# Kernel tuning notes

Measured on AMD Instinct MI355X. Metric: run time of the kernel, lower is better.

Reference implementation:

```python
import jax, jax.numpy as jnp
import numpy as np

L_MAX = 3
N_MAX = 8
N_PSEUDO = 4
N_SPECIES = 4
CUTOFF = 5.0


def real_sph_harm(u):
    # u: [E,3] unit vectors -> real spherical harmonics, l=0..3, [E,16]
    x, y, z = u[:, 0], u[:, 1], u[:, 2]
    x2, y2, z2 = x * x, y * y, z * z
    Y = [
        0.28209479177387814 * jnp.ones_like(x),
        0.4886025119029199 * y,
        0.4886025119029199 * z,
        0.4886025119029199 * x,
        1.0925484305920792 * x * y,
        1.0925484305920792 * y * z,
        0.31539156525252005 * (3.0 * z2 - 1.0),
        1.0925484305920792 * x * z,
        0.5462742152960396 * (x2 - y2),
        0.5900435899266435 * y * (3.0 * x2 - y2),
        2.890611442640554 * x * y * z,
        0.4570457994644658 * y * (5.0 * z2 - 1.0),
        0.3731763325901154 * z * (5.0 * z2 - 3.0),
        0.4570457994644658 * x * (5.0 * z2 - 1.0),
        1.445305721320277 * z * (x2 - y2),
        0.5900435899266435 * x * (x2 - 3.0 * y2),
    ]
    return jnp.stack(Y, axis=-1)


def setup_inputs() -> dict:
    key = jax.random.key(0)
    k0, k1, k2, k3 = jax.random.split(key, 4)
    N, E = 20000, 320000
    positions = jax.random.normal(k0, (N, 3), jnp.float32) * 2.0
    cells = (30.0 * jnp.eye(3, dtype=jnp.float32))[None]  # [1,3,3]
    species = jax.random.randint(k1, (N,), 0, N_SPECIES)  # species indices
    edge_indices = jax.random.randint(k2, (2, E), 0, N)
    edge_shifts = jnp.zeros((E, 3), jnp.int32)
    species_embed = jax.random.normal(k3, (N_SPECIES, N_PSEUDO), jnp.float32)  # alchemical coupling
    radial_mu = jnp.linspace(0.0, CUTOFF, N_MAX).astype(jnp.float32)
    radial_sigma = jnp.full((1,), 0.6, jnp.float32)
    return {
        "positions": positions,
        "cells": cells,
        "species": species,
        "edge_indices": edge_indices,
        "edge_shifts": edge_shifts,
        "species_embed": species_embed,
        "radial_mu": radial_mu,
        "radial_sigma": radial_sigma,
    }


def reference(positions, cells, species, edge_indices, edge_shifts, species_embed, radial_mu, radial_sigma):
    i, j = edge_indices[0], edge_indices[1]
    # per-edge displacement with periodic shifts
    rij = positions[j] - positions[i] + edge_shifts.astype(positions.dtype) @ cells[0]  # [E,3]
    r = jnp.sqrt(jnp.sum(rij * rij, axis=-1) + 1e-12)  # [E]
    u = rij / r[:, None]
    # smooth cosine cutoff
    fcut = jnp.where(r < CUTOFF, 0.5 * (jnp.cos(jnp.pi * r / CUTOFF) + 1.0), 0.0)
    # radial expansion [E, n_max]
    sig = radial_sigma[0]
    R = jnp.exp(-((r[:, None] - radial_mu) ** 2) / (2.0 * sig * sig)) * fcut[:, None]
    # angular expansion [E, (l_max+1)^2]
    Y = real_sph_harm(u)
    # alchemical pseudo-species embedding of the neighbor species [E, P]
    ej = species_embed[species[j]]
    N = positions.shape[0]
    outs = []
    for l in range(L_MAX + 1):
        Yl = Y[:, l * l:(l + 1) * (l + 1)]  # [E, 2l+1]
        # per-edge spherical-expansion contribution, properties = (pseudo, n) flattened -> Q
        feat = jnp.einsum('em,ep,en->empn', Yl, ej, R).reshape(Yl.shape[0], 2 * l + 1, -1)
        # scatter edges to centers: c_{i,m,q}
        c = jax.ops.segment_sum(feat, i, num_segments=N)  # [N, 2l+1, Q]
        cg = (2 * l + 1) ** (-0.5)
        # power spectrum: cg * sum_m c_{imq} c_{imr}  -> [N, Q, Q]
        ps = cg * jnp.einsum('nmq,nmr->nqr', c, c)
        outs.append(ps.reshape(N, -1))
    return jnp.concatenate(outs, axis=-1)  # [N, sum_l Q^2] = [20000, 4096]
```

## Files before the change

kernel.cpp:

```cpp
#include <hip/hip_runtime.h>
#include <math.h>

#define NM       16
#define NQ       32
#define CUT      5.0f
#define CAP      96

typedef float v4f __attribute__((ext_vector_type(4)));

__global__ __launch_bounds__(256) void edge_bin_kernel(
    const float* __restrict__ pos,
    const float* __restrict__ cells,
    const int*   __restrict__ species,
    const int*   __restrict__ eidx,
    const int*   __restrict__ eshift,
    int*         __restrict__ counts,
    float4*      __restrict__ buckets,
    int E)
{
    const int e = blockIdx.x * blockDim.x + threadIdx.x;
    if (e >= E) return;

    const int i = eidx[e];
    const int j = eidx[E + e];

    float dx = pos[3 * j + 0] - pos[3 * i + 0];
    float dy = pos[3 * j + 1] - pos[3 * i + 1];
    float dz = pos[3 * j + 2] - pos[3 * i + 2];

    const int sx = eshift[3 * e + 0];
    const int sy = eshift[3 * e + 1];
    const int sz = eshift[3 * e + 2];
    dx += (float)sx * cells[0] + (float)sy * cells[3] + (float)sz * cells[6];
    dy += (float)sx * cells[1] + (float)sy * cells[4] + (float)sz * cells[7];
    dz += (float)sx * cells[2] + (float)sy * cells[5] + (float)sz * cells[8];

    const float r2 = dx * dx + dy * dy + dz * dz;
    if (r2 >= CUT * CUT) return;

    const int slot = atomicAdd(&counts[i], 1);
    if (slot < CAP)
        buckets[(size_t)i * CAP + slot] =
            make_float4(dx, dy, dz, __int_as_float(species[j]));
}

__global__ __launch_bounds__(256) void node_fused_kernel(
    const float4* __restrict__ buckets,
    const int*    __restrict__ counts,
    const float*  __restrict__ semb,
    const float*  __restrict__ mu,
    const float*  __restrict__ sigma,
    float*        __restrict__ out,
    int N)
{
    const int node = blockIdx.x;
    const int tid  = threadIdx.x;

    __shared__ float sY[64][17];
    __shared__ float sW[64][33];
    __shared__ __align__(16) float sc[NM * NQ];
    __shared__ float s_mu[8];
    __shared__ float s_semb[16];

    if (tid < 8)  s_mu[tid]   = mu[tid];
    if (tid < 16) s_semb[tid] = semb[tid];

    const float sig    = sigma[0];
    const float inv2s2 = -1.0f / (2.0f * sig * sig);

    const int cnt = min(counts[node], CAP);

    const int q  = tid & 31;
    const int m0 = tid >> 5;
    float acc0 = 0.0f, acc1 = 0.0f;

    for (int base = 0; base < cnt; base += 64) {
        const int nb = min(cnt - base, 64);
        __syncthreads();

        const int lane = tid & 63;
        const int half = tid >> 6;
        if (lane < nb && half < 2) {
            const float4 b = buckets[(size_t)node * CAP + base + lane];
            const float dx = b.x, dy = b.y, dz = b.z;
            const float r2 = dx * dx + dy * dy + dz * dz + 1e-12f;
            const float r  = sqrtf(r2);
            const float invr = 1.0f / r;
            if (half == 0) {
                const float x = dx * invr, y = dy * invr, z = dz * invr;
                const float x2 = x * x, y2 = y * y, z2 = z * z;
                float* Yr = sY[lane];
                Yr[0]  = 0.28209479177387814f;
                Yr[1]  = 0.4886025119029199f * y;
                Yr[2]  = 0.4886025119029199f * z;
                Yr[3]  = 0.4886025119029199f * x;
                Yr[4]  = 1.0925484305920792f * x * y;
                Yr[5]  = 1.0925484305920792f * y * z;
                Yr[6]  = 0.31539156525252005f * (3.0f * z2 - 1.0f);
                Yr[7]  = 1.0925484305920792f * x * z;
                Yr[8]  = 0.5462742152960396f * (x2 - y2);
                Yr[9]  = 0.5900435899266435f * y * (3.0f * x2 - y2);
                Yr[10] = 2.890611442640554f  * x * y * z;
                Yr[11] = 0.4570457994644658f * y * (5.0f * z2 - 1.0f);
                Yr[12] = 0.3731763325901154f * z * (5.0f * z2 - 3.0f);
                Yr[13] = 0.4570457994644658f * x * (5.0f * z2 - 1.0f);
                Yr[14] = 1.445305721320277f  * z * (x2 - y2);
                Yr[15] = 0.5900435899266435f * x * (x2 - 3.0f * y2);
            } else {
                const float fcut = 0.5f * (__cosf(0.62831853071795864f * r) + 1.0f);
                const int sj = __float_as_int(b.w);
                float R[8];
#pragma unroll
                for (int n = 0; n < 8; ++n) {
                    const float dr = r - s_mu[n];
                    R[n] = __expf(dr * dr * inv2s2) * fcut;
                }
                float* Wr = sW[lane];
#pragma unroll
                for (int p = 0; p < 4; ++p) {
                    const float ejp = s_semb[sj * 4 + p];
#pragma unroll
                    for (int n = 0; n < 8; ++n)
                        Wr[p * 8 + n] = ejp * R[n];
                }
            }
        }
        __syncthreads();

        for (int e = 0; e < nb; ++e) {
            const float w = sW[e][q];
            acc0 += sY[e][m0]     * w;
            acc1 += sY[e][m0 + 8] * w;
        }
    }

    __syncthreads();
    sc[m0 * NQ + q]       = acc0;
    sc[(m0 + 8) * NQ + q] = acc1;
    __syncthreads();

    const float cg[4] = {1.0f, 0.57735026918962576f,
                         0.44721359549995794f, 0.37796447300922723f};
    const int qc = tid >> 3;
    const int r8 = tid & 7;

    const v4f* sc4 = (const v4f*)sc;
    v4f* op = (v4f*)out + (size_t)node * 1024;

#pragma unroll
    for (int l = 0; l < 4; ++l) {
        const int mb = l * l;
        const int mc = 2 * l + 1;
        v4f s = {0.0f, 0.0f, 0.0f, 0.0f};
        for (int m = 0; m < mc; ++m) {
            const float a  = sc[(mb + m) * NQ + qc];
            const v4f   bv = sc4[(mb + m) * 8 + r8];
            s += a * bv;
        }
        s *= cg[l];
        __builtin_nontemporal_store(s, &op[l * 256 + tid]);
    }
}

extern "C" void kernel_launch(void* const* d_in, const int* in_sizes, int n_in,
                              void* d_out, int out_size, void* d_ws, size_t ws_size,
                              hipStream_t stream) {
    const float* pos     = (const float*)d_in[0];
    const float* cells   = (const float*)d_in[1];
    const int*   species = (const int*)  d_in[2];
    const int*   eidx    = (const int*)  d_in[3];
    const int*   eshift  = (const int*)  d_in[4];
    const float* semb    = (const float*)d_in[5];
    const float* mu      = (const float*)d_in[6];
    const float* sigma   = (const float*)d_in[7];
    float*       out     = (float*)d_out;

    const int N = in_sizes[0] / 3;
    const int E = in_sizes[3] / 2;

    float4* buckets = (float4*)d_ws;
    const size_t bucket_bytes = (size_t)N * CAP * sizeof(float4);
    int* counts = (int*)((char*)d_ws + bucket_bytes);

    hipMemsetAsync(counts, 0, (size_t)N * sizeof(int), stream);

    edge_bin_kernel<<<(E + 255) / 256, 256, 0, stream>>>(
        pos, cells, species, eidx, eshift, counts, buckets, E);

    node_fused_kernel<<<N, 256, 0, stream>>>(
        buckets, counts, semb, mu, sigma, out, N);
}
```

Baseline: 357.4 us.

## Map one wavefront per node and drop block-wide barriers in fused kernel

The node kernel now assigns one 64-lane wavefront to each node, with four nodes per 256-thread block, instead of a whole block per node. Each wave processes neighbours in chunks of 16. One lane per edge computes both the spherical harmonics and the radial/species weights into a per-wave LDS slot, and there is no __syncthreads. Accumulation uses vector registers, and the power-spectrum stage loads B rows into registers and reuses them across four output column groups. The goal is to remove barrier overhead and idle threads when nodes have few edges, at the cost of relying on implicit wave-level LDS ordering and running more of the work serially per lane.

```diff
diff --git a/kernel.cpp b/kernel.cpp
--- a/kernel.cpp
+++ b/kernel.cpp
@@ -5,6 +5,8 @@
 #define NQ       32
 #define CUT      5.0f
 #define CAP      96
+#define CHUNK    16
+#define SLOT     52
 
 typedef float v4f __attribute__((ext_vector_type(4)));
 
@@ -53,112 +55,118 @@
     float*        __restrict__ out,
     int N)
 {
-    const int node = blockIdx.x;
-    const int tid  = threadIdx.x;
-
-    __shared__ float sY[64][17];
-    __shared__ float sW[64][33];
-    __shared__ __align__(16) float sc[NM * NQ];
-    __shared__ float s_mu[8];
-    __shared__ float s_semb[16];
-
-    if (tid < 8)  s_mu[tid]   = mu[tid];
-    if (tid < 16) s_semb[tid] = semb[tid];
+    const int wid  = threadIdx.x >> 6;
+    const int lane = threadIdx.x & 63;
+    const int node = blockIdx.x * 4 + wid;
+    if (node >= N) return;
+
+    __shared__ __align__(16) float sE[4][CHUNK * SLOT];
+    float* wbase = sE[wid];
 
     const float sig    = sigma[0];
     const float inv2s2 = -1.0f / (2.0f * sig * sig);
 
     const int cnt = min(counts[node], CAP);
 
-    const int q  = tid & 31;
-    const int m0 = tid >> 5;
-    float acc0 = 0.0f, acc1 = 0.0f;
-
-    for (int base = 0; base < cnt; base += 64) {
-        const int nb = min(cnt - base, 64);
-        __syncthreads();
-
-        const int lane = tid & 63;
-        const int half = tid >> 6;
-        if (lane < nb && half < 2) {
+    const int q = lane & 31;
+    const int h = lane >> 5;
+    v4f acc0 = {0.f, 0.f, 0.f, 0.f};
+    v4f acc1 = {0.f, 0.f, 0.f, 0.f};
+
+    for (int base = 0; base < cnt; base += CHUNK) {
+        const int nb = min(cnt - base, CHUNK);
+
+        if (lane < nb) {
             const float4 b = buckets[(size_t)node * CAP + base + lane];
             const float dx = b.x, dy = b.y, dz = b.z;
             const float r2 = dx * dx + dy * dy + dz * dz + 1e-12f;
             const float r  = sqrtf(r2);
             const float invr = 1.0f / r;
-            if (half == 0) {
-                const float x = dx * invr, y = dy * invr, z = dz * invr;
-                const float x2 = x * x, y2 = y * y, z2 = z * z;
-                float* Yr = sY[lane];
-                Yr[0]  = 0.28209479177387814f;
-                Yr[1]  = 0.4886025119029199f * y;
-                Yr[2]  = 0.4886025119029199f * z;
-                Yr[3]  = 0.4886025119029199f * x;
-                Yr[4]  = 1.0925484305920792f * x * y;
-                Yr[5]  = 1.0925484305920792f * y * z;
-                Yr[6]  = 0.31539156525252005f * (3.0f * z2 - 1.0f);
-                Yr[7]  = 1.0925484305920792f * x * z;
-                Yr[8]  = 0.5462742152960396f * (x2 - y2);
-                Yr[9]  = 0.5900435899266435f * y * (3.0f * x2 - y2);
-                Yr[10] = 2.890611442640554f  * x * y * z;
-                Yr[11] = 0.4570457994644658f * y * (5.0f * z2 - 1.0f);
-                Yr[12] = 0.3731763325901154f * z * (5.0f * z2 - 3.0f);
-                Yr[13] = 0.4570457994644658f * x * (5.0f * z2 - 1.0f);
-                Yr[14] = 1.445305721320277f  * z * (x2 - y2);
-                Yr[15] = 0.5900435899266435f * x * (x2 - 3.0f * y2);
-            } else {
-                const float fcut = 0.5f * (__cosf(0.62831853071795864f * r) + 1.0f);
-                const int sj = __float_as_int(b.w);
-                float R[8];
-#pragma unroll
-                for (int n = 0; n < 8; ++n) {
-                    const float dr = r - s_mu[n];
-                    R[n] = __expf(dr * dr * inv2s2) * fcut;
-                }
-                float* Wr = sW[lane];
-#pragma unroll
-                for (int p = 0; p < 4; ++p) {
-                    const float ejp = s_semb[sj * 4 + p];
-#pragma unroll
-                    for (int n = 0; n < 8; ++n)
-                        Wr[p * 8 + n] = ejp * R[n];
-                }
+            const float x = dx * invr, y = dy * invr, z = dz * invr;
+            const float x2 = x * x, y2 = y * y, z2 = z * z;
+
+            v4f* slot4 = (v4f*)(wbase + lane * SLOT);
+            v4f Ya, Yb, Yc, Yd;
+            Ya[0] = 0.28209479177387814f;
+            Ya[1] = 0.4886025119029199f * y;
+            Ya[2] = 0.4886025119029199f * z;
+            Ya[3] = 0.4886025119029199f * x;
+            Yb[0] = 1.0925484305920792f * x * y;
+            Yb[1] = 1.0925484305920792f * y * z;
+            Yb[2] = 0.31539156525252005f * (3.0f * z2 - 1.0f);
+            Yb[3] = 1.0925484305920792f * x * z;
+            Yc[0] = 0.5462742152960396f * (x2 - y2);
+            Yc[1] = 0.5900435899266435f * y * (3.0f * x2 - y2);
+            Yc[2] = 2.890611442640554f  * x * y * z;
+            Yc[3] = 0.4570457994644658f * y * (5.0f * z2 - 1.0f);
+            Yd[0] = 0.3731763325901154f * z * (5.0f * z2 - 3.0f);
+            Yd[1] = 0.4570457994644658f * x * (5.0f * z2 - 1.0f);
+            Yd[2] = 1.445305721320277f  * z * (x2 - y2);
+            Yd[3] = 0.5900435899266435f * x * (x2 - 3.0f * y2);
+            slot4[0] = Ya; slot4[1] = Yb; slot4[2] = Yc; slot4[3] = Yd;
+
+            const float fcut = 0.5f * (__cosf(0.62831853071795864f * r) + 1.0f);
+            float Rf[8];
+#pragma unroll
+            for (int n = 0; n < 8; ++n) {
+                const float dr = r - mu[n];
+                Rf[n] = __expf(dr * dr * inv2s2) * fcut;
+            }
+            const int sj = __float_as_int(b.w);
+#pragma unroll
+            for (int p = 0; p < 4; ++p) {
+                const float ejp = semb[sj * 4 + p];
+                v4f w0, w1;
+#pragma unroll
+                for (int n = 0; n < 4; ++n) { w0[n] = ejp * Rf[n]; w1[n] = ejp * Rf[4 + n]; }
+                slot4[4 + 2 * p]     = w0;
+                slot4[4 + 2 * p + 1] = w1;
             }
         }
-        __syncthreads();
 
         for (int e = 0; e < nb; ++e) {
-            const float w = sW[e][q];
-            acc0 += sY[e][m0]     * w;
-            acc1 += sY[e][m0 + 8] * w;
+            const float* ed = wbase + e * SLOT;
+            const float w  = ed[16 + q];
+            const v4f y0 = *(const v4f*)(ed + h * 8);
+            const v4f y1 = *(const v4f*)(ed + h * 8 + 4);
+            acc0 += y0 * w;
+            acc1 += y1 * w;
         }
     }
 
-    __syncthreads();
-    sc[m0 * NQ + q]       = acc0;
-    sc[(m0 + 8) * NQ + q] = acc1;
-    __syncthreads();
+    float* wc = wbase;
+#pragma unroll
+    for (int jj = 0; jj < 4; ++jj) {
+        wc[(h * 8 + jj) * NQ + q]     = acc0[jj];
+        wc[(h * 8 + 4 + jj) * NQ + q] = acc1[jj];
+    }
 
     const float cg[4] = {1.0f, 0.57735026918962576f,
                          0.44721359549995794f, 0.37796447300922723f};
-    const int qc = tid >> 3;
-    const int r8 = tid & 7;
-
-    const v4f* sc4 = (const v4f*)sc;
+    const v4f* wc4 = (const v4f*)wbase;
+    const int  r4  = lane & 7;
+    const int  qh  = lane >> 3;
     v4f* op = (v4f*)out + (size_t)node * 1024;
 
 #pragma unroll
     for (int l = 0; l < 4; ++l) {
         const int mb = l * l;
         const int mc = 2 * l + 1;
-        v4f s = {0.0f, 0.0f, 0.0f, 0.0f};
-        for (int m = 0; m < mc; ++m) {
-            const float a  = sc[(mb + m) * NQ + qc];
-            const v4f   bv = sc4[(mb + m) * 8 + r8];
-            s += a * bv;
+        v4f bv[7];
+#pragma unroll
+        for (int m = 0; m < 7; ++m)
+            if (m < mc) bv[m] = wc4[(mb + m) * 8 + r4];
+        const float cgl = cg[l];
+#pragma unroll
+        for (int k = 0; k < 4; ++k) {
+            const int q2 = k * 8 + qh;
+            v4f s = {0.f, 0.f, 0.f, 0.f};
+#pragma unroll
+            for (int m = 0; m < 7; ++m)
+                if (m < mc) s += wc[(mb + m) * NQ + q2] * bv[m];
+            s *= cgl;
+            __builtin_nontemporal_store(s, &op[l * 256 + k * 64 + lane]);
         }
-        s *= cg[l];
-        __builtin_nontemporal_store(s, &op[l * 256 + tid]);
     }
 }
 
@@ -187,6 +195,6 @@
     edge_bin_kernel<<<(E + 255) / 256, 256, 0, stream>>>(
         pos, cells, species, eidx, eshift, counts, buckets, E);
 
-    node_fused_kernel<<<N, 256, 0, stream>>>(
+    node_fused_kernel<<<(N + 3) / 4, 256, 0, stream>>>(
         buckets, counts, semb, mu, sigma, out, N);
 }
```

Result: slower. 367.0 us (+2.7%).
